# Performance work log

Hardware: AMD Instinct MI355X
Metric: run time of the kernel (lower is better)

## Reference

```python
import jax, jax.numpy as jnp
import numpy as np

VOCAB = 32000
HIDDEN = 1024
BATCH = 32
SEQ = 128


def setup_inputs() -> dict:
    key = jax.random.key(0)
    ks = jax.random.split(key, 8)
    p = lambda k, shape: (jax.random.normal(k, shape, dtype=jnp.float32) * 0.01)
    return {
        "x": jax.random.randint(ks[0], (BATCH, SEQ), 0, VOCAB, dtype=jnp.int64),
        "state": jnp.zeros((BATCH, HIDDEN), dtype=jnp.float32),
        "W_xr": p(ks[1], (VOCAB, HIDDEN)),
        "W_hr": p(ks[2], (HIDDEN, HIDDEN)),
        "b_r": jnp.zeros((HIDDEN,), dtype=jnp.float32),
        "W_xz": p(ks[3], (VOCAB, HIDDEN)),
        "W_hz": p(ks[4], (HIDDEN, HIDDEN)),
        "b_z": jnp.zeros((HIDDEN,), dtype=jnp.float32),
        "W_xh": p(ks[5], (VOCAB, HIDDEN)),
        "W_hh": p(ks[6], (HIDDEN, HIDDEN)),
        "b_h": jnp.zeros((HIDDEN,), dtype=jnp.float32),
        "W_ho": p(ks[7], (HIDDEN, VOCAB)),
        "b_o": jnp.zeros((VOCAB,), dtype=jnp.float32),
    }


def reference(x, state, W_xr, W_hr, b_r, W_xz, W_hz, b_z, W_xh, W_hh, b_h, W_ho, b_o):
    # x: (B, T) int tokens -> transpose to (T, B) like torch `x.T`.
    # one_hot(tok) @ W_x* is mathematically an embedding row gather: W_x*[tok].
    tokens = x.T  # (T, B)

    def step(h, tok):
        xr = W_xr[tok]  # (B, H)
        xz = W_xz[tok]
        xh = W_xh[tok]
        r = jax.nn.sigmoid(xr + h @ W_hr + b_r)
        z = jax.nn.sigmoid(xz + h @ W_hz + b_z)
        cand = jnp.tanh(xh + (r * h) @ W_hh + b_h)
        h_new = z * h + (1.0 - z) * cand
        out = h_new @ W_ho + b_o  # (B, V)
        return h_new, out

    final_state, outs = jax.lax.scan(step, state, tokens)  # outs: (T, B, V)
    # torch.cat(outputs, dim=0) concatenates per-step (B, V) blocks -> (T*B, V)
    return outs.reshape(-1, outs.shape[-1]), final_state
```

## Files before the change

kernel.cpp:

```cpp
#include <hip/hip_runtime.h>
#include <hip/hip_bf16.h>
#include <cstdint>
#include <cstddef>

#define VOCAB 32000
#define HIDDEN 1024
#define BATCH 32
#define SEQ 128

typedef __attribute__((ext_vector_type(8))) short short8v;
typedef __attribute__((ext_vector_type(4))) float float4v;
typedef __attribute__((ext_vector_type(2))) unsigned int uint2v;

__device__ __forceinline__ unsigned short f2bf(float f) {
    unsigned int x = __float_as_uint(f);
    unsigned int r = x + 0x7fffu + ((x >> 16) & 1u);
    return (unsigned short)(r >> 16);
}

__global__ __launch_bounds__(256) void k_prep(const float* __restrict__ who, unsigned short* __restrict__ bt,
                                              const float* __restrict__ whr, unsigned short* __restrict__ wrt,
                                              const float* __restrict__ whz, unsigned short* __restrict__ wzt,
                                              const float* __restrict__ whh, unsigned short* __restrict__ wht,
                                              const float* __restrict__ state, unsigned short* __restrict__ hinit) {
    __shared__ float tile[64][65];
    const int b = blockIdx.x;
    const int t = threadIdx.x;
    const float* in;
    unsigned short* outp;
    int cols, jb, kb;
    if (b < 8000) {
        in = who; outp = bt; cols = VOCAB; jb = b % 500; kb = b / 500;
    } else if (b < 8256) {
        int q = b - 8000; in = whr; outp = wrt; cols = HIDDEN; jb = q & 15; kb = q >> 4;
    } else if (b < 8512) {
        int q = b - 8256; in = whz; outp = wzt; cols = HIDDEN; jb = q & 15; kb = q >> 4;
    } else if (b < 8768) {
        int q = b - 8512; in = whh; outp = wht; cols = HIDDEN; jb = q & 15; kb = q >> 4;
    } else {
        int i = (b - 8768) * 256 + t;
        if (i < BATCH * HIDDEN) hinit[i] = f2bf(state[i]);
        return;
    }
    const int c  = t & 63;
    const int r0 = (t >> 6) * 16;
#pragma unroll
    for (int i = 0; i < 16; i++) {
        int r = r0 + i;
        tile[r][c] = in[(size_t)(kb * 64 + r) * cols + jb * 64 + c];
    }
    __syncthreads();
#pragma unroll
    for (int i = 0; i < 16; i++) {
        int r = r0 + i;
        outp[(size_t)(jb * 64 + r) * HIDDEN + kb * 64 + c] = f2bf(tile[c][r]);
    }
}


#define WAIT_VM0 asm volatile("s_waitcnt vmcnt(0)" ::: "memory")
#define LGKM0    asm volatile("s_waitcnt lgkmcnt(0)" ::: "memory")

#define ST8_WT(P, V) \
    asm volatile("global_store_dwordx2 %0, %1, off sc0 sc1" ::"v"(P), "v"(V) : "memory")

__device__ __forceinline__ void row_poll(const unsigned int* row, unsigned int tag) {
    const unsigned int* p = row + (threadIdx.x & 63);
    unsigned int a = __hip_atomic_load(p, __ATOMIC_RELAXED, __HIP_MEMORY_SCOPE_AGENT);
    int guard = 0;
    while (true) {
        unsigned int b = __hip_atomic_load(p, __ATOMIC_RELAXED, __HIP_MEMORY_SCOPE_AGENT);
        if (__all((int)(a >= tag))) break;
        a = __hip_atomic_load(p, __ATOMIC_RELAXED, __HIP_MEMORY_SCOPE_AGENT);
        if (__all((int)(b >= tag))) break;
        if (++guard > 8192) break;
    }
}

__global__ __launch_bounds__(64, 1) void k_rnn(const int* __restrict__ x,
                                               const float* __restrict__ state,
                                               const unsigned short* __restrict__ wrt,
                                               const unsigned short* __restrict__ wzt,
                                               const unsigned short* __restrict__ wht,
                                               const float* __restrict__ W_xr, const float* __restrict__ b_r,
                                               const float* __restrict__ W_xz, const float* __restrict__ b_z,
                                               const float* __restrict__ W_xh, const float* __restrict__ b_h,
                                               const unsigned short* __restrict__ hinit,
                                               unsigned short* __restrict__ hall,
                                               unsigned short* __restrict__ rhall,
                                               float* __restrict__ hstate_out,
                                               unsigned int* __restrict__ mbox) {
    const int bid = blockIdx.x;
    const int g   = bid >> 6;
    const int jsl = bid & 63;
    const int j0  = jsl * 16;
    const int b0  = g * 16;
    const int l   = threadIdx.x;
    const int llo = l & 15;
    const int lhi = l >> 4;
    const int jg  = j0 + llo;

    unsigned int* gm           = mbox + g * 64 * 64;
    const unsigned int* myrow  = gm + jsl * 64;
    unsigned int* pushtgt      = gm + l * 64 + jsl;

    __shared__ short8v wlds[3][32][64];
    __shared__ int xs[16 * SEQ];
    __shared__ unsigned short pack[16 * 16];

#pragma unroll
    for (int i = 0; i < 32; i++) {
        const size_t off = (size_t)jg * HIDDEN + i * 32 + lhi * 8;
        wlds[0][i][l] = *(const short8v*)&wrt[off];
        wlds[1][i][l] = *(const short8v*)&wzt[off];
        wlds[2][i][l] = *(const short8v*)&wht[off];
    }
    for (int i = l; i < 16 * SEQ; i += 64)
        xs[i] = x[(size_t)(b0 + (i >> 7)) * SEQ + (i & 127)];

    const float brv = b_r[jg], bzv = b_z[jg], bhv = b_h[jg];
    float4v hO;
#pragma unroll
    for (int q = 0; q < 4; q++) hO[q] = state[(b0 + 4 * lhi + q) * HIDDEN + jg];
    LGKM0;

    for (int t = 0; t < SEQ; t++) {
        const unsigned short* hprev =
            t ? (hall + (size_t)(t - 1) * BATCH * HIDDEN) : hinit;
        unsigned short* rhp = rhall + (size_t)t * BATCH * HIDDEN;
        unsigned short* hp  = hall + (size_t)t * BATCH * HIDDEN;

        int tok[4];
#pragma unroll
        for (int q = 0; q < 4; q++) tok[q] = xs[(4 * lhi + q) * SEQ + t];
        float xr[4], xz[4], xh[4];
#pragma unroll
        for (int q = 0; q < 4; q++) {
            xr[q] = W_xr[(size_t)tok[q] * HIDDEN + jg];
            xz[q] = W_xz[(size_t)tok[q] * HIDDEN + jg];
            xh[q] = W_xh[(size_t)tok[q] * HIDDEN + jg];
        }

        if (t) row_poll(myrow, 2u * (unsigned)t);

        short8v af[32];
#pragma unroll
        for (int i = 0; i < 32; i++)
            af[i] = *(const short8v*)&hprev[(b0 + llo) * HIDDEN + i * 32 + lhi * 8];

        float4v aR0 = {0.f, 0.f, 0.f, 0.f}, aR1 = {0.f, 0.f, 0.f, 0.f};
        float4v aZ0 = {0.f, 0.f, 0.f, 0.f}, aZ1 = {0.f, 0.f, 0.f, 0.f};
#pragma unroll
        for (int i = 0; i < 32; i += 2) {
            aR0 = __builtin_amdgcn_mfma_f32_16x16x32_bf16(af[i],     wlds[0][i][l],     aR0, 0, 0, 0);
            aZ0 = __builtin_amdgcn_mfma_f32_16x16x32_bf16(af[i],     wlds[1][i][l],     aZ0, 0, 0, 0);
            aR1 = __builtin_amdgcn_mfma_f32_16x16x32_bf16(af[i + 1], wlds[0][i + 1][l], aR1, 0, 0, 0);
            aZ1 = __builtin_amdgcn_mfma_f32_16x16x32_bf16(af[i + 1], wlds[1][i + 1][l], aZ1, 0, 0, 0);
        }

        float4v zv;
#pragma unroll
        for (int q = 0; q < 4; q++) {
            float sr = aR0[q] + aR1[q] + xr[q] + brv;
            float sz = aZ0[q] + aZ1[q] + xz[q] + bzv;
            float rv = 1.f / (1.f + __expf(-sr));
            zv[q]    = 1.f / (1.f + __expf(-sz));
            pack[(4 * lhi + q) * 16 + llo] = f2bf(rv * hO[q]);
        }
        LGKM0;
        __builtin_amdgcn_wave_barrier();
        {
            uint2v v = *(const uint2v*)&pack[(l >> 2) * 16 + (l & 3) * 4];
            ST8_WT(&rhp[(b0 + (l >> 2)) * HIDDEN + j0 + (l & 3) * 4], v);
            WAIT_VM0;
            __hip_atomic_store(pushtgt, 2u * (unsigned)t + 1u, __ATOMIC_RELAXED,
                               __HIP_MEMORY_SCOPE_AGENT);
        }

        row_poll(myrow, 2u * (unsigned)t + 1u);

        short8v ar[32];
#pragma unroll
        for (int i = 0; i < 32; i++)
            ar[i] = *(const short8v*)&rhp[(b0 + llo) * HIDDEN + i * 32 + lhi * 8];

        float4v aC0 = {0.f, 0.f, 0.f, 0.f}, aC1 = {0.f, 0.f, 0.f, 0.f};
#pragma unroll
        for (int i = 0; i < 32; i += 2) {
            aC0 = __builtin_amdgcn_mfma_f32_16x16x32_bf16(ar[i],     wlds[2][i][l],     aC0, 0, 0, 0);
            aC1 = __builtin_amdgcn_mfma_f32_16x16x32_bf16(ar[i + 1], wlds[2][i + 1][l], aC1, 0, 0, 0);
        }
#pragma unroll
        for (int q = 0; q < 4; q++) {
            float a = aC0[q] + aC1[q] + xh[q] + bhv;
            a = fminf(15.f, fmaxf(-15.f, a));
            float e2   = __expf(2.f * a);
            float cand = (e2 - 1.f) / (e2 + 1.f);
            float hn   = zv[q] * hO[q] + (1.f - zv[q]) * cand;
            hO[q]      = hn;
            pack[(4 * lhi + q) * 16 + llo] = f2bf(hn);
        }
        LGKM0;
        __builtin_amdgcn_wave_barrier();
        {
            uint2v v = *(const uint2v*)&pack[(l >> 2) * 16 + (l & 3) * 4];
            ST8_WT(&hp[(b0 + (l >> 2)) * HIDDEN + j0 + (l & 3) * 4], v);
            WAIT_VM0;
            __hip_atomic_store(pushtgt, 2u * (unsigned)t + 2u, __ATOMIC_RELAXED,
                               __HIP_MEMORY_SCOPE_AGENT);
        }
    }

#pragma unroll
    for (int q = 0; q < 4; q++)
        hstate_out[(b0 + 4 * lhi + q) * HIDDEN + jg] = hO[q];
}

#define GTM 16
#define GTN 125

__device__ __forceinline__ void gload_lds16(const void* g, void* l) {
    __builtin_amdgcn_global_load_lds((const __attribute__((address_space(1))) void*)g,
                                     (__attribute__((address_space(3))) void*)l, 16, 0, 0);
}

__device__ __forceinline__ void stage_half(const unsigned short* __restrict__ mbase,
                                           unsigned short* ldsm, int half, int isB,
                                           int kt, int tid) {
#pragma unroll
    for (int i = 0; i < 2; i++) {
        int s  = i * 512 + tid;
        int ri = s >> 3;
        int cb = (s & 7) * 16;
        int rt = isB ? ((ri >> 5) * 64 + half * 32 + (ri & 31))
                     : ((ri >> 6) * 128 + half * 64 + (ri & 63));
        int cbs = cb ^ ((rt & 7) << 4);
        gload_lds16(mbase + (size_t)rt * HIDDEN + kt * 64 + (cbs >> 1),
                    ldsm + rt * 64 + (cb >> 1));
    }
}

__global__ __launch_bounds__(512, 2) void k_gemm8(const unsigned short* __restrict__ A,
                                                  const unsigned short* __restrict__ B,
                                                  const float* __restrict__ bo,
                                                  float* __restrict__ out) {
    __shared__ unsigned short lds[2][2][256 * 64];

    const int wg   = blockIdx.x;
    const int swz  = (wg & 7) * 250 + (wg >> 3);
    const int mb   = swz / GTN;
    const int nb   = swz % GTN;
    const int row0 = mb * 256, col0 = nb * 256;

    const int tid = threadIdx.x;
    const int w   = tid >> 6;
    const int wm  = w >> 2;
    const int wn  = w & 3;
    const int l   = tid & 63;
    const int llo = l & 15;
    const int lhi = l >> 4;

    const unsigned short* Ab = A + (size_t)row0 * HIDDEN;
    const unsigned short* Bb = B + (size_t)col0 * HIDDEN;

    float4v acc[8][4];
#pragma unroll
    for (int i = 0; i < 8; i++)
#pragma unroll
        for (int j = 0; j < 4; j++) acc[i][j] = float4v{0.f, 0.f, 0.f, 0.f};

    stage_half(Ab, &lds[0][0][0], 0, 0, 0, tid);
    stage_half(Bb, &lds[0][1][0], 0, 1, 0, tid);
    stage_half(Ab, &lds[0][0][0], 1, 0, 0, tid);
    stage_half(Bb, &lds[0][1][0], 1, 1, 0, tid);
    stage_half(Ab, &lds[1][0][0], 0, 0, 1, tid);
    stage_half(Bb, &lds[1][1][0], 0, 1, 1, tid);
    asm volatile("s_waitcnt vmcnt(4)" ::: "memory");
    __builtin_amdgcn_s_barrier();

    for (int kt = 0; kt < 16; kt++) {
        unsigned short* lA = &lds[kt & 1][0][0];
        unsigned short* lB = &lds[kt & 1][1][0];
        unsigned short* nA = &lds[(kt & 1) ^ 1][0][0];
        unsigned short* nB = &lds[(kt & 1) ^ 1][1][0];
        short8v afr[4][2];
        short8v bfr[2][2][2];

#pragma unroll
        for (int mfq = 0; mfq < 4; mfq++)
#pragma unroll
            for (int ks = 0; ks < 2; ks++) {
                int rt = wm * 128 + mfq * 16 + llo;
                int cb = ks * 64 + lhi * 16;
                afr[mfq][ks] = *(const short8v*)&lA[rt * 64 + ((cb ^ ((rt & 7) << 4)) >> 1)];
            }
#pragma unroll
        for (int nfq = 0; nfq < 2; nfq++)
#pragma unroll
            for (int ks = 0; ks < 2; ks++) {
                int rt = wn * 64 + nfq * 16 + llo;
                int cb = ks * 64 + lhi * 16;
                bfr[0][nfq][ks] = *(const short8v*)&lB[rt * 64 + ((cb ^ ((rt & 7) << 4)) >> 1)];
            }
        if (kt + 1 < 16) stage_half(Ab, nA, 1, 0, kt + 1, tid);
        __builtin_amdgcn_s_barrier();
        __builtin_amdgcn_s_setprio(1);
#pragma unroll
        for (int mfq = 0; mfq < 4; mfq++)
#pragma unroll
            for (int nfq = 0; nfq < 2; nfq++)
#pragma unroll
                for (int ks = 0; ks < 2; ks++)
                    acc[mfq][nfq] = __builtin_amdgcn_mfma_f32_16x16x32_bf16(
                        afr[mfq][ks], bfr[0][nfq][ks], acc[mfq][nfq], 0, 0, 0);
        __builtin_amdgcn_s_setprio(0);
        __builtin_amdgcn_s_barrier();

#pragma unroll
        for (int nfq = 0; nfq < 2; nfq++)
#pragma unroll
            for (int ks = 0; ks < 2; ks++) {
                int rt = wn * 64 + 32 + nfq * 16 + llo;
                int cb = ks * 64 + lhi * 16;
                bfr[1][nfq][ks] = *(const short8v*)&lB[rt * 64 + ((cb ^ ((rt & 7) << 4)) >> 1)];
            }
        if (kt + 1 < 16) stage_half(Bb, nB, 1, 1, kt + 1, tid);
        __builtin_amdgcn_s_barrier();
        __builtin_amdgcn_s_setprio(1);
#pragma unroll
        for (int mfq = 0; mfq < 4; mfq++)
#pragma unroll
            for (int nfq = 0; nfq < 2; nfq++)
#pragma unroll
                for (int ks = 0; ks < 2; ks++)
                    acc[mfq][2 + nfq] = __builtin_amdgcn_mfma_f32_16x16x32_bf16(
                        afr[mfq][ks], bfr[1][nfq][ks], acc[mfq][2 + nfq], 0, 0, 0);
        __builtin_amdgcn_s_setprio(0);
        __builtin_amdgcn_s_barrier();

#pragma unroll
        for (int mfq = 0; mfq < 4; mfq++)
#pragma unroll
            for (int ks = 0; ks < 2; ks++) {
                int rt = wm * 128 + 64 + mfq * 16 + llo;
                int cb = ks * 64 + lhi * 16;
                afr[mfq][ks] = *(const short8v*)&lA[rt * 64 + ((cb ^ ((rt & 7) << 4)) >> 1)];
            }
        if (kt + 2 < 16) stage_half(Ab, lA, 0, 0, kt + 2, tid);
        __builtin_amdgcn_s_barrier();
        __builtin_amdgcn_s_setprio(1);
#pragma unroll
        for (int mfq = 0; mfq < 4; mfq++)
#pragma unroll
            for (int nfq = 0; nfq < 2; nfq++)
#pragma unroll
                for (int ks = 0; ks < 2; ks++)
                    acc[4 + mfq][nfq] = __builtin_amdgcn_mfma_f32_16x16x32_bf16(
                        afr[mfq][ks], bfr[0][nfq][ks], acc[4 + mfq][nfq], 0, 0, 0);
        __builtin_amdgcn_s_setprio(0);
        __builtin_amdgcn_s_barrier();

        if (kt + 2 < 16) stage_half(Bb, lB, 0, 1, kt + 2, tid);
        __builtin_amdgcn_s_barrier();
        __builtin_amdgcn_s_setprio(1);
#pragma unroll
        for (int mfq = 0; mfq < 4; mfq++)
#pragma unroll
            for (int nfq = 0; nfq < 2; nfq++)
#pragma unroll
                for (int ks = 0; ks < 2; ks++)
                    acc[4 + mfq][2 + nfq] = __builtin_amdgcn_mfma_f32_16x16x32_bf16(
                        afr[mfq][ks], bfr[1][nfq][ks], acc[4 + mfq][2 + nfq], 0, 0, 0);
        __builtin_amdgcn_s_setprio(0);
        if (kt + 2 < 16) {
            asm volatile("s_waitcnt vmcnt(4)" ::: "memory");
        } else if (kt + 1 < 16) {
            asm volatile("s_waitcnt vmcnt(0)" ::: "memory");
        }
        __builtin_amdgcn_s_barrier();
    }

#pragma unroll
    for (int mf = 0; mf < 8; mf++) {
        int grow = row0 + wm * 128 + mf * 16 + lhi * 4;
#pragma unroll
        for (int nf = 0; nf < 4; nf++) {
            int gcol   = col0 + wn * 64 + nf * 16 + llo;
            float bias = bo[gcol];
#pragma unroll
            for (int r = 0; r < 4; r++)
                __builtin_nontemporal_store(acc[mf][nf][r] + bias,
                                            &out[(size_t)(grow + r) * VOCAB + gcol]);
        }
    }
}


extern "C" void kernel_launch(void* const* d_in, const int* in_sizes, int n_in,
                              void* d_out, int out_size, void* d_ws, size_t ws_size,
                              hipStream_t stream) {
    const int*   x     = (const int*)d_in[0];
    const float* state = (const float*)d_in[1];
    const float* W_xr  = (const float*)d_in[2];
    const float* W_hr  = (const float*)d_in[3];
    const float* b_r   = (const float*)d_in[4];
    const float* W_xz  = (const float*)d_in[5];
    const float* W_hz  = (const float*)d_in[6];
    const float* b_z   = (const float*)d_in[7];
    const float* W_xh  = (const float*)d_in[8];
    const float* W_hh  = (const float*)d_in[9];
    const float* b_h   = (const float*)d_in[10];
    const float* W_ho  = (const float*)d_in[11];
    const float* b_o   = (const float*)d_in[12];

    float* out    = (float*)d_out;
    float* hstate = out + (size_t)SEQ * BATCH * VOCAB;

    char* ws = (char*)d_ws;
    unsigned short* hall  = (unsigned short*)ws;
    unsigned short* rhall = (unsigned short*)(ws + 8388608);
    unsigned short* bt    = (unsigned short*)(ws + 16777216);
    unsigned short* wrt   = (unsigned short*)(ws + 82313216);
    unsigned short* wzt   = (unsigned short*)(ws + 84410368);
    unsigned short* wht   = (unsigned short*)(ws + 86507520);
    unsigned short* hinit = (unsigned short*)(ws + 88604672);
    unsigned int*   mbox  = (unsigned int*)(ws + 88670208);

    hipMemsetAsync(mbox, 0, 32768, stream);
    k_prep<<<8896, 256, 0, stream>>>(W_ho, bt, W_hr, wrt, W_hz, wzt, W_hh, wht, state, hinit);

    k_rnn<<<128, 64, 0, stream>>>(x, state, wrt, wzt, wht, W_xr, b_r, W_xz, b_z, W_xh, b_h,
                                  hinit, hall, rhall, hstate, mbox);

    k_gemm8<<<dim3(2000), 512, 0, stream>>>(hall, bt, b_o, out);
}
```

Before: 1.102 ms.

## Overlap W_ho bf16 transpose with the recurrent kernel using extra blocks

Moves the W_ho fp32-to-bf16 transposed conversion out of the prep kernel and into 500 extra blocks of the recurrent kernel. Those blocks run on CUs the 128 sequential RNN blocks leave idle, so the conversion overlaps the latency-bound recurrence instead of preceding it. The RNN kernel now launches 256-thread blocks and idles three of its four waves. The new transpose reads strided columns without an LDS tile, which gives less coalesced loads, and it may compete with the RNN blocks for memory bandwidth or scheduling.

```diff
diff --git a/kernel.cpp b/kernel.cpp
--- a/kernel.cpp
+++ b/kernel.cpp
@@ -18,42 +18,34 @@
     return (unsigned short)(r >> 16);
 }
 
-__global__ __launch_bounds__(256) void k_prep(const float* __restrict__ who, unsigned short* __restrict__ bt,
-                                              const float* __restrict__ whr, unsigned short* __restrict__ wrt,
+__global__ __launch_bounds__(256) void k_prep(const float* __restrict__ whr, unsigned short* __restrict__ wrt,
                                               const float* __restrict__ whz, unsigned short* __restrict__ wzt,
                                               const float* __restrict__ whh, unsigned short* __restrict__ wht,
                                               const float* __restrict__ state, unsigned short* __restrict__ hinit) {
-    __shared__ float tile[64][65];
     const int b = blockIdx.x;
     const int t = threadIdx.x;
-    const float* in;
-    unsigned short* outp;
-    int cols, jb, kb;
-    if (b < 8000) {
-        in = who; outp = bt; cols = VOCAB; jb = b % 500; kb = b / 500;
-    } else if (b < 8256) {
-        int q = b - 8000; in = whr; outp = wrt; cols = HIDDEN; jb = q & 15; kb = q >> 4;
-    } else if (b < 8512) {
-        int q = b - 8256; in = whz; outp = wzt; cols = HIDDEN; jb = q & 15; kb = q >> 4;
-    } else if (b < 8768) {
-        int q = b - 8512; in = whh; outp = wht; cols = HIDDEN; jb = q & 15; kb = q >> 4;
-    } else {
-        int i = (b - 8768) * 256 + t;
+    if (b >= 768) {
+        int i = (b - 768) * 256 + t;
         if (i < BATCH * HIDDEN) hinit[i] = f2bf(state[i]);
         return;
     }
+    __shared__ float tile[64][65];
+    const float* in    = (b < 256) ? whr : (b < 512) ? whz : whh;
+    unsigned short* op = (b < 256) ? wrt : (b < 512) ? wzt : wht;
+    const int q  = b & 255;
+    const int jb = q & 15, kb = q >> 4;
     const int c  = t & 63;
     const int r0 = (t >> 6) * 16;
 #pragma unroll
     for (int i = 0; i < 16; i++) {
         int r = r0 + i;
-        tile[r][c] = in[(size_t)(kb * 64 + r) * cols + jb * 64 + c];
+        tile[r][c] = in[(size_t)(kb * 64 + r) * HIDDEN + jb * 64 + c];
     }
     __syncthreads();
 #pragma unroll
     for (int i = 0; i < 16; i++) {
         int r = r0 + i;
-        outp[(size_t)(jb * 64 + r) * HIDDEN + kb * 64 + c] = f2bf(tile[c][r]);
+        op[(size_t)(jb * 64 + r) * HIDDEN + kb * 64 + c] = f2bf(tile[c][r]);
     }
 }
 
@@ -77,20 +69,41 @@
     }
 }
 
-__global__ __launch_bounds__(64, 1) void k_rnn(const int* __restrict__ x,
-                                               const float* __restrict__ state,
-                                               const unsigned short* __restrict__ wrt,
-                                               const unsigned short* __restrict__ wzt,
-                                               const unsigned short* __restrict__ wht,
-                                               const float* __restrict__ W_xr, const float* __restrict__ b_r,
-                                               const float* __restrict__ W_xz, const float* __restrict__ b_z,
-                                               const float* __restrict__ W_xh, const float* __restrict__ b_h,
-                                               const unsigned short* __restrict__ hinit,
-                                               unsigned short* __restrict__ hall,
-                                               unsigned short* __restrict__ rhall,
-                                               float* __restrict__ hstate_out,
-                                               unsigned int* __restrict__ mbox) {
+__global__ __launch_bounds__(256, 1) void k_rnn(const int* __restrict__ x,
+                                                const float* __restrict__ state,
+                                                const unsigned short* __restrict__ wrt,
+                                                const unsigned short* __restrict__ wzt,
+                                                const unsigned short* __restrict__ wht,
+                                                const float* __restrict__ W_xr, const float* __restrict__ b_r,
+                                                const float* __restrict__ W_xz, const float* __restrict__ b_z,
+                                                const float* __restrict__ W_xh, const float* __restrict__ b_h,
+                                                const unsigned short* __restrict__ hinit,
+                                                unsigned short* __restrict__ hall,
+                                                unsigned short* __restrict__ rhall,
+                                                float* __restrict__ hstate_out,
+                                                unsigned int* __restrict__ mbox,
+                                                const float* __restrict__ who,
+                                                unsigned short* __restrict__ bt) {
     const int bid = blockIdx.x;
+
+    __shared__ short8v wlds[3][32][64];
+    __shared__ int xs[16 * SEQ];
+    __shared__ unsigned short pack[16 * 16];
+
+    if (bid >= 128) {
+        const int n = (bid - 128) * 64 + (threadIdx.x & 63);
+        const int w4 = threadIdx.x >> 6;
+        for (int k0 = w4 * 256; k0 < w4 * 256 + 256; k0 += 8) {
+            short8v v;
+#pragma unroll
+            for (int e = 0; e < 8; e++)
+                v[e] = (short)f2bf(who[(size_t)(k0 + e) * VOCAB + n]);
+            *(short8v*)&bt[(size_t)n * HIDDEN + k0] = v;
+        }
+        return;
+    }
+    if (threadIdx.x >= 64) return;
+
     const int g   = bid >> 6;
     const int jsl = bid & 63;
     const int j0  = jsl * 16;
@@ -103,10 +116,6 @@
     unsigned int* gm           = mbox + g * 64 * 64;
     const unsigned int* myrow  = gm + jsl * 64;
     unsigned int* pushtgt      = gm + l * 64 + jsl;
-
-    __shared__ short8v wlds[3][32][64];
-    __shared__ int xs[16 * SEQ];
-    __shared__ unsigned short pack[16 * 16];
 
 #pragma unroll
     for (int i = 0; i < 32; i++) {
@@ -427,10 +436,10 @@
     unsigned int*   mbox  = (unsigned int*)(ws + 88670208);
 
     hipMemsetAsync(mbox, 0, 32768, stream);
-    k_prep<<<8896, 256, 0, stream>>>(W_ho, bt, W_hr, wrt, W_hz, wzt, W_hh, wht, state, hinit);
-
-    k_rnn<<<128, 64, 0, stream>>>(x, state, wrt, wzt, wht, W_xr, b_r, W_xz, b_z, W_xh, b_h,
-                                  hinit, hall, rhall, hstate, mbox);
+    k_prep<<<896, 256, 0, stream>>>(W_hr, wrt, W_hz, wzt, W_hh, wht, state, hinit);
+
+    k_rnn<<<628, 256, 0, stream>>>(x, state, wrt, wzt, wht, W_xr, b_r, W_xz, b_z, W_xh, b_h,
+                                   hinit, hall, rhall, hstate, mbox, W_ho, bt);
 
     k_gemm8<<<dim3(2000), 512, 0, stream>>>(hall, bt, b_o, out);
 }
```

Result: no change. 1.082 ms (-1.9%).
